# Kernel optimization log

Measured on AMD Instinct MI355X. Metric: run time of the kernel, lower is better.

## Reference

```python
import jax, jax.numpy as jnp
import numpy as np

B, N, D = 64, 512, 128  # graphs per batch, max nodes per graph, hidden_dim


def setup_inputs() -> dict:
    key = jax.random.key(0)
    ks = jax.random.split(key, 9)
    h1 = jax.random.normal(ks[0], (B, N, D), jnp.float32)
    h2 = jax.random.normal(ks[1], (B, N, D), jnp.float32)
    s = 1.0 / np.sqrt(D)
    Wk = jax.random.normal(ks[2], (D, D), jnp.float32) * s
    bk = jax.random.normal(ks[3], (D,), jnp.float32) * s
    Wq = jax.random.normal(ks[4], (D, D), jnp.float32) * s
    bq = jax.random.normal(ks[5], (D,), jnp.float32) * s
    t = jnp.asarray(np.sqrt(1.0 / D), jnp.float32)  # self.t = sqrt(1/hidden_dim)
    len1 = jax.random.randint(ks[6], (B,), 1, N + 1, jnp.int32)
    len2 = jax.random.randint(ks[7], (B,), 1, N + 1, jnp.int32)
    return {"h1": h1, "h2": h2, "Wk": Wk, "bk": bk, "Wq": Wq, "bq": bq,
            "t": t, "len1": len1, "len2": len2}


def reference(h1, h2, Wk, bk, Wq, bq, t, len1, len2):
    # valid-node masks for the ragged (padded) graphs
    pos = jnp.arange(N)
    m1 = pos[None, :] < len1[:, None]  # [B, N]
    m2 = pos[None, :] < len2[:, None]  # [B, N]

    # k = Linear(h), q = Linear(h)  (torch Linear: x @ W.T + b)
    k1 = jnp.einsum('bnd,ed->bne', h1, Wk) + bk
    k2 = jnp.einsum('bnd,ed->bne', h2, Wk) + bk
    q1 = jnp.einsum('bnd,ed->bne', h1, Wq) + bq
    q2 = jnp.einsum('bnd,ed->bne', h2, Wq) + bq

    NEG = jnp.asarray(-1e9, h1.dtype)

    # g1 nodes attend over g2 nodes; note values == keys (k2)
    s1 = jnp.einsum('bnd,bmd->bnm', q1, k2) * t           # [B, N1, N2]
    s1 = jnp.where(m2[:, None, :], s1, NEG)
    a1 = jax.nn.softmax(s1, axis=-1)
    o1 = jnp.einsum('bnm,bmd->bnd', a1, k2) * m1[:, :, None]

    # g2 nodes attend over g1 nodes; values == k1
    s2 = jnp.einsum('bnd,bmd->bnm', q2, k1) * t           # [B, N2, N1]
    s2 = jnp.where(m1[:, None, :], s2, NEG)
    a2 = jax.nn.softmax(s2, axis=-1)
    o2 = jnp.einsum('bnm,bmd->bnd', a2, k1) * m2[:, :, None]

    return o1, o2
```

## Files before the change

kernel.cpp:

```cpp
#include <hip/hip_runtime.h>

typedef __attribute__((ext_vector_type(8))) short bf16x8;
typedef __attribute__((ext_vector_type(4))) short s16x4;
typedef __attribute__((ext_vector_type(4))) float f32x4;
typedef __attribute__((ext_vector_type(4))) int   i32x4;

#define MFMA16 __builtin_amdgcn_mfma_f32_16x16x32_bf16

#define B_ 64
#define N_ 512
#define D_ 128
#define KBUF_ 16384

__device__ __forceinline__ unsigned short f2bf(float f) {
  unsigned u = __builtin_bit_cast(unsigned, f);
  u += 0x7fffu + ((u >> 16) & 1u);
  return (unsigned short)(u >> 16);
}
__device__ __forceinline__ int packbf2(float lo, float hi) {
  return (int)((unsigned)f2bf(lo) | ((unsigned)f2bf(hi) << 16));
}

__device__ __forceinline__ void gload_lds16(const void* g, void* l) {
  __builtin_amdgcn_global_load_lds((const __attribute__((address_space(1))) unsigned*)g,
                                   (__attribute__((address_space(3))) unsigned*)l, 16, 0, 0);
}

__global__ void prep_w(const float* __restrict__ Wk, const float* __restrict__ Wq,
                       short* __restrict__ wkb, short* __restrict__ wqb) {
  int i = blockIdx.x * 256 + threadIdx.x;
  if (i < D_ * D_) { wkb[i] = (short)f2bf(Wk[i]); wqb[i] = (short)f2bf(Wq[i]); }
}

__global__ __launch_bounds__(256, 2) void proj_kernel(
    const float* __restrict__ h1, const float* __restrict__ h2,
    const short* __restrict__ wkb, const short* __restrict__ wqb,
    const float* __restrict__ bk, const float* __restrict__ bq,
    short* __restrict__ k1, short* __restrict__ k2,
    short* __restrict__ q1, short* __restrict__ q2,
    short* __restrict__ k1T, short* __restrict__ k2T) {
  const int wave = threadIdx.x >> 6, lane = threadIdx.x & 63;
  const int c = lane & 15, g = lane >> 4;
  const int rw = blockIdx.x * 128 + wave * 32;
  const int inp = rw >> 15;
  const int loc = rw & 32767;
  const int b = loc >> 9, n0 = loc & 511;
  const float* __restrict__ h = inp ? h2 : h1;
  short* __restrict__ kout = inp ? k2 : k1;
  short* __restrict__ qout = inp ? q2 : q1;
  short* __restrict__ kT   = inp ? k2T : k1T;

  bf16x8 xf[2][4];
#pragma unroll
  for (int mt = 0; mt < 2; ++mt) {
    const float* hr = h + (long)(loc + mt * 16 + c) * D_;
#pragma unroll
    for (int kk = 0; kk < 4; ++kk) {
      f32x4 lo = *(const f32x4*)(hr + kk * 32 + g * 8);
      f32x4 hi = *(const f32x4*)(hr + kk * 32 + g * 8 + 4);
      bf16x8 v;
      v[0] = (short)f2bf(lo[0]); v[1] = (short)f2bf(lo[1]);
      v[2] = (short)f2bf(lo[2]); v[3] = (short)f2bf(lo[3]);
      v[4] = (short)f2bf(hi[0]); v[5] = (short)f2bf(hi[1]);
      v[6] = (short)f2bf(hi[2]); v[7] = (short)f2bf(hi[3]);
      xf[mt][kk] = v;
    }
  }

#pragma unroll
  for (int et = 0; et < 8; ++et) {
    bf16x8 wkf[4], wqf[4];
    const short* wkr = wkb + (et * 16 + c) * D_;
    const short* wqr = wqb + (et * 16 + c) * D_;
#pragma unroll
    for (int kk = 0; kk < 4; ++kk) {
      wkf[kk] = *(const bf16x8*)(wkr + kk * 32 + g * 8);
      wqf[kk] = *(const bf16x8*)(wqr + kk * 32 + g * 8);
    }
    f32x4 ak[2], aq[2], at[2];
#pragma unroll
    for (int mt = 0; mt < 2; ++mt) {
      ak[mt] = (f32x4){0.f, 0.f, 0.f, 0.f};
      aq[mt] = (f32x4){0.f, 0.f, 0.f, 0.f};
      at[mt] = (f32x4){0.f, 0.f, 0.f, 0.f};
    }
#pragma unroll
    for (int kk = 0; kk < 4; ++kk) {
#pragma unroll
      for (int mt = 0; mt < 2; ++mt) {
        ak[mt] = MFMA16(wkf[kk], xf[mt][kk], ak[mt], 0, 0, 0);
        aq[mt] = MFMA16(wqf[kk], xf[mt][kk], aq[mt], 0, 0, 0);
        at[mt] = MFMA16(xf[mt][kk], wkf[kk], at[mt], 0, 0, 0);
      }
    }
    f32x4 bkv = *(const f32x4*)(bk + et * 16 + g * 4);
    f32x4 bqv = *(const f32x4*)(bq + et * 16 + g * 4);
    float bks = bk[et * 16 + c];
#pragma unroll
    for (int mt = 0; mt < 2; ++mt) {
      s16x4 pk, pq, pt;
#pragma unroll
      for (int j = 0; j < 4; ++j) {
        pk[j] = (short)f2bf(ak[mt][j] + bkv[j]);
        pq[j] = (short)f2bf(aq[mt][j] + bqv[j]);
        pt[j] = (short)f2bf(at[mt][j] + bks);
      }
      long row = (long)(loc + mt * 16 + c);
      *(s16x4*)(kout + row * D_ + et * 16 + g * 4) = pk;
      *(s16x4*)(qout + row * D_ + et * 16 + g * 4) = pq;
      *(s16x4*)(kT + ((long)(b * D_ + et * 16 + c)) * N_ + n0 + mt * 16 + g * 4) = pt;
    }
  }
}

__global__ __launch_bounds__(256, 2) void attn_kernel(
    const short* __restrict__ k1, const short* __restrict__ k2,
    const short* __restrict__ q1, const short* __restrict__ q2,
    const short* __restrict__ k1T, const short* __restrict__ k2T,
    const float* __restrict__ tptr,
    const int* __restrict__ len1, const int* __restrict__ len2,
    float* __restrict__ out) {
  extern __shared__ char smem[];
  const int tid = threadIdx.x;
  const int wave = tid >> 6, lane = tid & 63;
  const int c = lane & 15, g = lane >> 4;
  const int wgid = blockIdx.x;
  const int qt = wgid >> 7;
  const int bd = wgid & 127;
  const int dir = bd >> 6, b = bd & 63;
  const short* __restrict__ qp = dir ? q2 : q1;
  const short* __restrict__ kp = dir ? k1 : k2;
  const short* __restrict__ vT = dir ? k1T : k2T;
  const int lk = dir ? len1[b] : len2[b];
  const int lq = dir ? len2[b] : len1[b];
  float* __restrict__ o = out + (long)dir * B_ * N_ * D_;
  const float ts = *tptr;
  const int q0 = qt * 64 + wave * 16;

  const char* kbase = (const char*)(kp + (long)b * N_ * D_);
  const char* vbase = (const char*)(vT + (long)b * D_ * N_);

  auto stage = [&](int i) {
    char* buf = smem + KBUF_ * (i % 3);
    if (i < 8) {
#pragma unroll
      for (int j = 0; j < 4; ++j) {
        int L = j * 4096 + tid * 16;
        int row = L >> 8, off = L & 255;
        const char* gp = kbase + (i * 64 + row) * 256 + (off ^ ((row & 7) << 4));
        gload_lds16(gp, buf + j * 4096 + (wave << 10));
      }
    } else {
      int ch = i - 8;
#pragma unroll
      for (int j = 0; j < 4; ++j) {
        int L = j * 4096 + tid * 16;
        int row = L >> 7, off = L & 127;
        const char* gp = vbase + row * 1024 + ch * 128 + (off ^ ((row & 7) << 4));
        gload_lds16(gp, buf + j * 4096 + (wave << 10));
      }
    }
  };

  bf16x8 qf[4];
  const short* qrow = qp + ((long)(b * N_ + q0 + c)) * D_;
#pragma unroll
  for (int kk = 0; kk < 4; ++kk) qf[kk] = *(const bf16x8*)(qrow + kk * 32 + g * 8);

  stage(0);
  stage(1);

  f32x4 s[32];
#pragma unroll
  for (int ch = 0; ch < 8; ++ch) {
    asm volatile("s_waitcnt vmcnt(4)" ::: "memory");
    __builtin_amdgcn_sched_barrier(0);
    __builtin_amdgcn_s_barrier();
    __builtin_amdgcn_sched_barrier(0);
    stage(ch + 2);
    const char* buf = smem + KBUF_ * (ch % 3);
    __builtin_amdgcn_s_setprio(1);
#pragma unroll
    for (int tl = 0; tl < 4; ++tl) {
      int r = tl * 16 + c;
      const char* base = buf + (r << 8);
      int sw = (r & 7) << 4;
      f32x4 acc = (f32x4){0.f, 0.f, 0.f, 0.f};
#pragma unroll
      for (int kk = 0; kk < 4; ++kk) {
        bf16x8 kf = *(const bf16x8*)(base + ((kk * 64 + g * 16) ^ sw));
        acc = MFMA16(kf, qf[kk], acc, 0, 0, 0);
      }
      const int node = ch * 64 + tl * 16 + g * 4;
#pragma unroll
      for (int j = 0; j < 4; ++j) {
        float v = acc[j] * ts;
        s[ch * 4 + tl][j] = (node + j < lk) ? v : -1e9f;
      }
    }
    __builtin_amdgcn_s_setprio(0);
  }

  float mx = -3e38f;
#pragma unroll
  for (int t16 = 0; t16 < 32; ++t16)
#pragma unroll
    for (int j = 0; j < 4; ++j) mx = fmaxf(mx, s[t16][j]);
  mx = fmaxf(mx, __shfl_xor(mx, 16));
  mx = fmaxf(mx, __shfl_xor(mx, 32));
  float rs = 0.f;
#pragma unroll
  for (int t16 = 0; t16 < 32; ++t16)
#pragma unroll
    for (int j = 0; j < 4; ++j) {
      float p = __expf(s[t16][j] - mx);
      s[t16][j] = p;
      rs += p;
    }
  rs += __shfl_xor(rs, 16);
  rs += __shfl_xor(rs, 32);
  const float rinv = 1.0f / rs;

  f32x4 oacc[8];
#pragma unroll
  for (int dt = 0; dt < 8; ++dt) oacc[dt] = (f32x4){0.f, 0.f, 0.f, 0.f};
  const int srcA = c + ((g & 1) << 5);
  const int srcB = srcA + 16;
  const bool lowhalf = (g < 2);
#pragma unroll
  for (int ch = 0; ch < 8; ++ch) {
    if (ch == 7) asm volatile("s_waitcnt vmcnt(0)" ::: "memory");
    else         asm volatile("s_waitcnt vmcnt(4)" ::: "memory");
    __builtin_amdgcn_sched_barrier(0);
    __builtin_amdgcn_s_barrier();
    __builtin_amdgcn_sched_barrier(0);
    if (ch + 10 < 16) stage(ch + 10);
    const char* buf = smem + KBUF_ * ((ch + 8) % 3);
#pragma unroll
    for (int q = 0; q < 2; ++q) {
      int t0 = ch * 4 + 2 * q;
      int a0 = packbf2(s[t0][0], s[t0][1]);
      int a1 = packbf2(s[t0][2], s[t0][3]);
      int b0 = packbf2(s[t0 + 1][0], s[t0 + 1][1]);
      int b1 = packbf2(s[t0 + 1][2], s[t0 + 1][3]);
      int xa0 = __shfl(a0, srcA), xb0 = __shfl(b0, srcA);
      int xa1 = __shfl(a1, srcA), xb1 = __shfl(b1, srcA);
      int ya0 = __shfl(a0, srcB), yb0 = __shfl(b0, srcB);
      int ya1 = __shfl(a1, srcB), yb1 = __shfl(b1, srcB);
      i32x4 ui;
      ui[0] = lowhalf ? xa0 : xb0;
      ui[1] = lowhalf ? xa1 : xb1;
      ui[2] = lowhalf ? ya0 : yb0;
      ui[3] = lowhalf ? ya1 : yb1;
      bf16x8 pf = __builtin_bit_cast(bf16x8, ui);
      __builtin_amdgcn_s_setprio(1);
#pragma unroll
      for (int dt = 0; dt < 8; ++dt) {
        int row = dt * 16 + c;
        bf16x8 vt = *(const bf16x8*)(buf + row * 128 + ((q * 64 + g * 16) ^ ((row & 7) << 4)));
        oacc[dt] = MFMA16(vt, pf, oacc[dt], 0, 0, 0);
      }
      __builtin_amdgcn_s_setprio(0);
    }
  }

  const int qg = q0 + c;
  const bool valid = qg < lq;
  float* orow = o + ((long)(b * N_ + qg)) * D_;
#pragma unroll
  for (int dt = 0; dt < 8; ++dt) {
    f32x4 vo;
#pragma unroll
    for (int j = 0; j < 4; ++j) vo[j] = valid ? oacc[dt][j] * rinv : 0.0f;
    *(f32x4*)(orow + dt * 16 + g * 4) = vo;
  }
}

extern "C" void kernel_launch(void* const* d_in, const int* in_sizes, int n_in,
                              void* d_out, int out_size, void* d_ws, size_t ws_size,
                              hipStream_t stream) {
  const float* h1 = (const float*)d_in[0];
  const float* h2 = (const float*)d_in[1];
  const float* Wk = (const float*)d_in[2];
  const float* bk = (const float*)d_in[3];
  const float* Wq = (const float*)d_in[4];
  const float* bq = (const float*)d_in[5];
  const float* t  = (const float*)d_in[6];
  const int* len1 = (const int*)d_in[7];
  const int* len2 = (const int*)d_in[8];

  char* ws = (char*)d_ws;
  const size_t SZ = (size_t)B_ * N_ * D_ * 2;
  short* k1  = (short*)(ws + 0 * SZ);
  short* k2  = (short*)(ws + 1 * SZ);
  short* q1  = (short*)(ws + 2 * SZ);
  short* q2  = (short*)(ws + 3 * SZ);
  short* k1T = (short*)(ws + 4 * SZ);
  short* k2T = (short*)(ws + 5 * SZ);
  short* wkb = (short*)(ws + 6 * SZ);
  short* wqb = (short*)(ws + 6 * SZ + D_ * D_ * 2);

  prep_w<<<64, 256, 0, stream>>>(Wk, Wq, wkb, wqb);
  proj_kernel<<<512, 256, 0, stream>>>(h1, h2, wkb, wqb, bk, bq,
                                       k1, k2, q1, q2, k1T, k2T);
  attn_kernel<<<1024, 256, 3 * KBUF_, stream>>>(k1, k2, q1, q2, k1T, k2T,
                                                t, len1, len2, (float*)d_out);
}
```

Before: 75.94 us.

## Switch attention to online-softmax flash loop with 2 waves and 32 queries per wave

Replaces the two-pass attention (all scores held in registers, then softmax, then PV) with a single streaming loop over 16 chunks of 32 keys. Each chunk loads its K and V^T slices together into a double buffer and applies online softmax with a lazy rescale that only fires when the running max grows by more than a threshold. Each wave now handles two 16-query tiles so every K/V LDS fragment feeds two MFMAs, and the block shrinks to 128 threads with static 32KB LDS. This removes the large score register array and halves K/V LDS reads per query. The cost is per-chunk reductions, shuffles and exp work, a full vmcnt(0) wait each iteration with only one stage of prefetch, and fewer waves per block.

```diff
diff --git a/kernel.cpp b/kernel.cpp
--- a/kernel.cpp
+++ b/kernel.cpp
@@ -10,7 +10,8 @@
 #define B_ 64
 #define N_ 512
 #define D_ 128
-#define KBUF_ 16384
+#define NCHK 16
+#define BUFB 16384
 
 __device__ __forceinline__ unsigned short f2bf(float f) {
   unsigned u = __builtin_bit_cast(unsigned, f);
@@ -113,14 +114,14 @@
   }
 }
 
-__global__ __launch_bounds__(256, 2) void attn_kernel(
+__global__ __launch_bounds__(128, 2) void attn_kernel(
     const short* __restrict__ k1, const short* __restrict__ k2,
     const short* __restrict__ q1, const short* __restrict__ q2,
     const short* __restrict__ k1T, const short* __restrict__ k2T,
     const float* __restrict__ tptr,
     const int* __restrict__ len1, const int* __restrict__ len2,
     float* __restrict__ out) {
-  extern __shared__ char smem[];
+  __shared__ char smem[2 * BUFB];
   const int tid = threadIdx.x;
   const int wave = tid >> 6, lane = tid & 63;
   const int c = lane & 15, g = lane >> 4;
@@ -135,114 +136,123 @@
   const int lq = dir ? len2[b] : len1[b];
   float* __restrict__ o = out + (long)dir * B_ * N_ * D_;
   const float ts = *tptr;
-  const int q0 = qt * 64 + wave * 16;
+  const int q0 = qt * 64 + wave * 32;
 
   const char* kbase = (const char*)(kp + (long)b * N_ * D_);
   const char* vbase = (const char*)(vT + (long)b * D_ * N_);
 
   auto stage = [&](int i) {
-    char* buf = smem + KBUF_ * (i % 3);
-    if (i < 8) {
-#pragma unroll
-      for (int j = 0; j < 4; ++j) {
-        int L = j * 4096 + tid * 16;
-        int row = L >> 8, off = L & 255;
-        const char* gp = kbase + (i * 64 + row) * 256 + (off ^ ((row & 7) << 4));
-        gload_lds16(gp, buf + j * 4096 + (wave << 10));
-      }
-    } else {
-      int ch = i - 8;
-#pragma unroll
-      for (int j = 0; j < 4; ++j) {
-        int L = j * 4096 + tid * 16;
-        int row = L >> 7, off = L & 127;
-        const char* gp = vbase + row * 1024 + ch * 128 + (off ^ ((row & 7) << 4));
-        gload_lds16(gp, buf + j * 4096 + (wave << 10));
-      }
+    char* buf = smem + BUFB * (i & 1);
+#pragma unroll
+    for (int j = 0; j < 4; ++j) {
+      int L = j * 2048 + tid * 16;
+      int row = L >> 8, off = L & 255;
+      const char* gp = kbase + (i * 32 + row) * 256 + (off ^ ((row & 7) << 4));
+      gload_lds16(gp, buf + j * 2048 + (wave << 10));
+    }
+#pragma unroll
+    for (int j = 0; j < 4; ++j) {
+      int L = j * 2048 + tid * 16;
+      int row = L >> 6, off = L & 63;
+      const char* gp = vbase + row * 1024 + i * 64 + (off ^ (((row >> 1) & 3) << 4));
+      gload_lds16(gp, buf + 8192 + j * 2048 + (wave << 10));
     }
   };
 
-  bf16x8 qf[4];
-  const short* qrow = qp + ((long)(b * N_ + q0 + c)) * D_;
-#pragma unroll
-  for (int kk = 0; kk < 4; ++kk) qf[kk] = *(const bf16x8*)(qrow + kk * 32 + g * 8);
+  bf16x8 qf[2][4];
+#pragma unroll
+  for (int t = 0; t < 2; ++t) {
+    const short* qrow = qp + ((long)(b * N_ + q0 + t * 16 + c)) * D_;
+#pragma unroll
+    for (int kk = 0; kk < 4; ++kk) qf[t][kk] = *(const bf16x8*)(qrow + kk * 32 + g * 8);
+  }
+
+  f32x4 oacc[2][8];
+#pragma unroll
+  for (int t = 0; t < 2; ++t)
+#pragma unroll
+    for (int dt = 0; dt < 8; ++dt) oacc[t][dt] = (f32x4){0.f, 0.f, 0.f, 0.f};
+  float m[2] = {-3e38f, -3e38f};
+  float l[2] = {0.f, 0.f};
+
+  const int srcA = c + ((g & 1) << 5);
+  const int srcB = srcA + 16;
+  const bool lowhalf = (g < 2);
 
   stage(0);
-  stage(1);
-
-  f32x4 s[32];
-#pragma unroll
-  for (int ch = 0; ch < 8; ++ch) {
-    asm volatile("s_waitcnt vmcnt(4)" ::: "memory");
+
+#pragma unroll 2
+  for (int ch = 0; ch < NCHK; ++ch) {
+    asm volatile("s_waitcnt vmcnt(0)" ::: "memory");
     __builtin_amdgcn_sched_barrier(0);
     __builtin_amdgcn_s_barrier();
     __builtin_amdgcn_sched_barrier(0);
-    stage(ch + 2);
-    const char* buf = smem + KBUF_ * (ch % 3);
+    if (ch + 1 < NCHK) stage(ch + 1);
+    const char* buf = smem + BUFB * (ch & 1);
+
+    f32x4 sv[2][2];
     __builtin_amdgcn_s_setprio(1);
 #pragma unroll
-    for (int tl = 0; tl < 4; ++tl) {
+    for (int tl = 0; tl < 2; ++tl) {
       int r = tl * 16 + c;
       const char* base = buf + (r << 8);
       int sw = (r & 7) << 4;
-      f32x4 acc = (f32x4){0.f, 0.f, 0.f, 0.f};
+      f32x4 a0 = (f32x4){0.f, 0.f, 0.f, 0.f};
+      f32x4 a1 = (f32x4){0.f, 0.f, 0.f, 0.f};
 #pragma unroll
       for (int kk = 0; kk < 4; ++kk) {
         bf16x8 kf = *(const bf16x8*)(base + ((kk * 64 + g * 16) ^ sw));
-        acc = MFMA16(kf, qf[kk], acc, 0, 0, 0);
-      }
-      const int node = ch * 64 + tl * 16 + g * 4;
-#pragma unroll
-      for (int j = 0; j < 4; ++j) {
-        float v = acc[j] * ts;
-        s[ch * 4 + tl][j] = (node + j < lk) ? v : -1e9f;
-      }
+        a0 = MFMA16(kf, qf[0][kk], a0, 0, 0, 0);
+        a1 = MFMA16(kf, qf[1][kk], a1, 0, 0, 0);
+      }
+      sv[0][tl] = a0; sv[1][tl] = a1;
     }
     __builtin_amdgcn_s_setprio(0);
-  }
-
-  float mx = -3e38f;
-#pragma unroll
-  for (int t16 = 0; t16 < 32; ++t16)
-#pragma unroll
-    for (int j = 0; j < 4; ++j) mx = fmaxf(mx, s[t16][j]);
-  mx = fmaxf(mx, __shfl_xor(mx, 16));
-  mx = fmaxf(mx, __shfl_xor(mx, 32));
-  float rs = 0.f;
-#pragma unroll
-  for (int t16 = 0; t16 < 32; ++t16)
-#pragma unroll
-    for (int j = 0; j < 4; ++j) {
-      float p = __expf(s[t16][j] - mx);
-      s[t16][j] = p;
-      rs += p;
-    }
-  rs += __shfl_xor(rs, 16);
-  rs += __shfl_xor(rs, 32);
-  const float rinv = 1.0f / rs;
-
-  f32x4 oacc[8];
-#pragma unroll
-  for (int dt = 0; dt < 8; ++dt) oacc[dt] = (f32x4){0.f, 0.f, 0.f, 0.f};
-  const int srcA = c + ((g & 1) << 5);
-  const int srcB = srcA + 16;
-  const bool lowhalf = (g < 2);
-#pragma unroll
-  for (int ch = 0; ch < 8; ++ch) {
-    if (ch == 7) asm volatile("s_waitcnt vmcnt(0)" ::: "memory");
-    else         asm volatile("s_waitcnt vmcnt(4)" ::: "memory");
-    __builtin_amdgcn_sched_barrier(0);
-    __builtin_amdgcn_s_barrier();
-    __builtin_amdgcn_sched_barrier(0);
-    if (ch + 10 < 16) stage(ch + 10);
-    const char* buf = smem + KBUF_ * ((ch + 8) % 3);
-#pragma unroll
-    for (int q = 0; q < 2; ++q) {
-      int t0 = ch * 4 + 2 * q;
-      int a0 = packbf2(s[t0][0], s[t0][1]);
-      int a1 = packbf2(s[t0][2], s[t0][3]);
-      int b0 = packbf2(s[t0 + 1][0], s[t0 + 1][1]);
-      int b1 = packbf2(s[t0 + 1][2], s[t0 + 1][3]);
+
+    bf16x8 pf[2];
+#pragma unroll
+    for (int t = 0; t < 2; ++t) {
+      float pmax = -3e38f;
+#pragma unroll
+      for (int tl = 0; tl < 2; ++tl) {
+        const int node = ch * 32 + tl * 16 + g * 4;
+#pragma unroll
+        for (int j = 0; j < 4; ++j) {
+          float v = sv[t][tl][j] * ts;
+          v = (node + j < lk) ? v : -1e9f;
+          sv[t][tl][j] = v;
+          pmax = fmaxf(pmax, v);
+        }
+      }
+      pmax = fmaxf(pmax, __shfl_xor(pmax, 16));
+      pmax = fmaxf(pmax, __shfl_xor(pmax, 32));
+      if (!__all(pmax - m[t] <= 8.0f)) {
+        float newm = fmaxf(m[t], pmax);
+        float sc = __expf(m[t] - newm);
+        m[t] = newm;
+        l[t] *= sc;
+#pragma unroll
+        for (int dt = 0; dt < 8; ++dt)
+#pragma unroll
+          for (int j = 0; j < 4; ++j) oacc[t][dt][j] *= sc;
+      }
+      float sum = 0.f;
+#pragma unroll
+      for (int tl = 0; tl < 2; ++tl)
+#pragma unroll
+        for (int j = 0; j < 4; ++j) {
+          float p = __expf(sv[t][tl][j] - m[t]);
+          sv[t][tl][j] = p;
+          sum += p;
+        }
+      sum += __shfl_xor(sum, 16);
+      sum += __shfl_xor(sum, 32);
+      l[t] += sum;
+
+      int a0 = packbf2(sv[t][0][0], sv[t][0][1]);
+      int a1 = packbf2(sv[t][0][2], sv[t][0][3]);
+      int b0 = packbf2(sv[t][1][0], sv[t][1][1]);
+      int b1 = packbf2(sv[t][1][2], sv[t][1][3]);
       int xa0 = __shfl(a0, srcA), xb0 = __shfl(b0, srcA);
       int xa1 = __shfl(a1, srcA), xb1 = __shfl(b1, srcA);
       int ya0 = __shfl(a0, srcB), yb0 = __shfl(b0, srcB);
@@ -252,27 +262,34 @@
       ui[1] = lowhalf ? xa1 : xb1;
       ui[2] = lowhalf ? ya0 : yb0;
       ui[3] = lowhalf ? ya1 : yb1;
-      bf16x8 pf = __builtin_bit_cast(bf16x8, ui);
-      __builtin_amdgcn_s_setprio(1);
-#pragma unroll
-      for (int dt = 0; dt < 8; ++dt) {
-        int row = dt * 16 + c;
-        bf16x8 vt = *(const bf16x8*)(buf + row * 128 + ((q * 64 + g * 16) ^ ((row & 7) << 4)));
-        oacc[dt] = MFMA16(vt, pf, oacc[dt], 0, 0, 0);
-      }
-      __builtin_amdgcn_s_setprio(0);
-    }
-  }
-
-  const int qg = q0 + c;
-  const bool valid = qg < lq;
-  float* orow = o + ((long)(b * N_ + qg)) * D_;
-#pragma unroll
-  for (int dt = 0; dt < 8; ++dt) {
-    f32x4 vo;
-#pragma unroll
-    for (int j = 0; j < 4; ++j) vo[j] = valid ? oacc[dt][j] * rinv : 0.0f;
-    *(f32x4*)(orow + dt * 16 + g * 4) = vo;
+      pf[t] = __builtin_bit_cast(bf16x8, ui);
+    }
+
+    __builtin_amdgcn_s_setprio(1);
+#pragma unroll
+    for (int dt = 0; dt < 8; ++dt) {
+      int row = dt * 16 + c;
+      const char* vb = buf + 8192 + row * 64;
+      bf16x8 vt = *(const bf16x8*)(vb + ((g * 16) ^ (((row >> 1) & 3) << 4)));
+      oacc[0][dt] = MFMA16(vt, pf[0], oacc[0][dt], 0, 0, 0);
+      oacc[1][dt] = MFMA16(vt, pf[1], oacc[1][dt], 0, 0, 0);
+    }
+    __builtin_amdgcn_s_setprio(0);
+  }
+
+#pragma unroll
+  for (int t = 0; t < 2; ++t) {
+    const int qg = q0 + t * 16 + c;
+    const bool valid = qg < lq;
+    const float rinv = 1.0f / l[t];
+    float* orow = o + ((long)(b * N_ + qg)) * D_;
+#pragma unroll
+    for (int dt = 0; dt < 8; ++dt) {
+      f32x4 vo;
+#pragma unroll
+      for (int j = 0; j < 4; ++j) vo[j] = valid ? oacc[t][dt][j] * rinv : 0.0f;
+      *(f32x4*)(orow + dt * 16 + g * 4) = vo;
+    }
   }
 }
 
@@ -303,6 +320,6 @@
   prep_w<<<64, 256, 0, stream>>>(Wk, Wq, wkb, wqb);
   proj_kernel<<<512, 256, 0, stream>>>(h1, h2, wkb, wqb, bk, bq,
                                        k1, k2, q1, q2, k1T, k2T);
-  attn_kernel<<<1024, 256, 3 * KBUF_, stream>>>(k1, k2, q1, q2, k1T, k2T,
-                                                t, len1, len2, (float*)d_out);
-}
+  attn_kernel<<<1024, 128, 0, stream>>>(k1, k2, q1, q2, k1T, k2T,
+                                        t, len1, len2, (float*)d_out);
+}
```

Result: no change. 76.56 us (+0.8%).
